# Optimization experiments

Hardware: AMD Instinct MI355X
Metric: run time of the kernel (lower is better)

The kernel has to match this reference:

```python
import jax, jax.numpy as jnp
import numpy as np

N_NODES = 100000
N_EDGES = 1600000
D_FEAT = 64


def setup_inputs() -> dict:
    key = jax.random.key(0)
    k1, k2, k3, k4 = jax.random.split(key, 4)
    x = jax.random.normal(k1, (N_NODES, D_FEAT), dtype=jnp.float32)
    edge_values = jax.random.uniform(k2, (N_EDGES,), dtype=jnp.float32)
    # row-sorted targets mimic a coalesced sparse COO matrix
    target_index = jnp.sort(jax.random.randint(k3, (N_EDGES,), 0, N_NODES, dtype=jnp.int32))
    source_index = jax.random.randint(k4, (N_EDGES,), 0, N_NODES, dtype=jnp.int32)
    return {"x": x, "edge_values": edge_values,
            "target_index": target_index, "source_index": source_index}


def reference(x, edge_values, target_index, source_index):
    # sparsify_message: gather source rows -> [n_edges, d]
    msg = x[source_index]
    # scale by sparse neighborhood values
    msg = edge_values[:, None] * msg
    # aggregate: scatter-sum into target cells -> [n_nodes, d]
    out = jax.ops.segment_sum(msg, target_index, num_segments=N_NODES)
    return out
```

## Files before the change

kernel.cpp:

```cpp
#include <hip/hip_runtime.h>

#define N_NODES 100000
#define N_EDGES 1600000
#define D_FEAT 64

__global__ __launch_bounds__(256) void build_row_ptr(
    const int* __restrict__ tgt, int* __restrict__ row_ptr)
{
    int e = blockIdx.x * blockDim.x + threadIdx.x;
    if (e >= N_EDGES) return;
    int cur = tgt[e];
    int lo  = (e == 0) ? 0 : tgt[e - 1] + 1;
    for (int n = lo; n <= cur; ++n) row_ptr[n] = e;
    if (e == N_EDGES - 1) {
        for (int n = cur + 1; n <= N_NODES; ++n) row_ptr[n] = N_EDGES;
    }
}

__global__ __launch_bounds__(256) void gather_sum(
    const float4* __restrict__ x4,
    const float*  __restrict__ ev,
    const int*    __restrict__ src,
    const int*    __restrict__ row_ptr,
    float4*       __restrict__ out4)
{
    const int node = blockIdx.x * 4 + (threadIdx.x >> 6);
    if (node >= N_NODES) return;
    const int lane = threadIdx.x & 63;
    const int g    = lane >> 4;
    const int f    = lane & 15;

    const int start = row_ptr[node];
    const int end   = row_ptr[node + 1];

    float4 acc = make_float4(0.f, 0.f, 0.f, 0.f);
    for (int e0 = start; e0 < end; e0 += 4) {
        const int  e     = e0 + g;
        const bool valid = (e < end);
        const int  es    = valid ? e : start;
        const float w    = valid ? ev[es] : 0.0f;
        const int   s    = src[es];
        const float4 v   = x4[s * 16 + f];
        acc.x = fmaf(w, v.x, acc.x);
        acc.y = fmaf(w, v.y, acc.y);
        acc.z = fmaf(w, v.z, acc.z);
        acc.w = fmaf(w, v.w, acc.w);
    }

    acc.x += __shfl_xor(acc.x, 16, 64);
    acc.y += __shfl_xor(acc.y, 16, 64);
    acc.z += __shfl_xor(acc.z, 16, 64);
    acc.w += __shfl_xor(acc.w, 16, 64);
    acc.x += __shfl_xor(acc.x, 32, 64);
    acc.y += __shfl_xor(acc.y, 32, 64);
    acc.z += __shfl_xor(acc.z, 32, 64);
    acc.w += __shfl_xor(acc.w, 32, 64);

    if (g == 0) out4[node * 16 + f] = acc;
}

extern "C" void kernel_launch(void* const* d_in, const int* in_sizes, int n_in,
                              void* d_out, int out_size, void* d_ws, size_t ws_size,
                              hipStream_t stream) {
    const float* x            = (const float*)d_in[0];
    const float* edge_values  = (const float*)d_in[1];
    const int*   target_index = (const int*)d_in[2];
    const int*   source_index = (const int*)d_in[3];
    float*       out          = (float*)d_out;
    int*         row_ptr      = (int*)d_ws;

    build_row_ptr<<<(N_EDGES + 255) / 256, 256, 0, stream>>>(target_index, row_ptr);

    gather_sum<<<(N_NODES + 3) / 4, 256, 0, stream>>>(
        (const float4*)x, edge_values, source_index, row_ptr, (float4*)out);
}
```

Baseline: 148.0 us.

## Process four nodes per 16-lane group with software-pipelined triple-buffered gathers

Each 16-lane group now handles four consecutive nodes as one contiguous edge range, walking the edges serially and flushing accumulators at row boundaries instead of splitting each node's edges across four lane groups and reducing with shuffles. Source indices, weights and x rows are prefetched two stages ahead in a rotating A/B/C register pipeline to hide gather latency. This removes the cross-lane shuffle reduction and the idle lanes on short rows. In exchange it raises register pressure and makes each group's work sequential, so per-thread memory parallelism depends on the prefetch depth.

```diff
diff --git a/kernel.cpp b/kernel.cpp
--- a/kernel.cpp
+++ b/kernel.cpp
@@ -24,39 +24,84 @@
     const int*    __restrict__ row_ptr,
     float4*       __restrict__ out4)
 {
-    const int node = blockIdx.x * 4 + (threadIdx.x >> 6);
-    if (node >= N_NODES) return;
-    const int lane = threadIdx.x & 63;
-    const int g    = lane >> 4;
-    const int f    = lane & 15;
+    const int gid = (blockIdx.x * 256 + threadIdx.x) >> 4;
+    if (gid >= N_NODES / 4) return;
+    const int f  = threadIdx.x & 15;
+    const int n0 = gid * 4;
 
-    const int start = row_ptr[node];
-    const int end   = row_ptr[node + 1];
+    const int rp0 = row_ptr[n0];
+    const int rp1 = row_ptr[n0 + 1];
+    const int rp2 = row_ptr[n0 + 2];
+    const int rp3 = row_ptr[n0 + 3];
+    const int rp4 = row_ptr[n0 + 4];
+
+    const int e0   = rp0;
+    const int eend = rp4;
+    const int len  = eend - e0;
 
     float4 acc = make_float4(0.f, 0.f, 0.f, 0.f);
-    for (int e0 = start; e0 < end; e0 += 4) {
-        const int  e     = e0 + g;
-        const bool valid = (e < end);
-        const int  es    = valid ? e : start;
-        const float w    = valid ? ev[es] : 0.0f;
-        const int   s    = src[es];
-        const float4 v   = x4[s * 16 + f];
-        acc.x = fmaf(w, v.x, acc.x);
-        acc.y = fmaf(w, v.y, acc.y);
-        acc.z = fmaf(w, v.z, acc.z);
-        acc.w = fmaf(w, v.w, acc.w);
+    int node  = n0;
+    int bound = rp1;
+
+    if (len > 0) {
+        const int emax = eend - 1;
+
+#define LOADSW(EIDX, S, W) do { int _e = (EIDX); int _ec = _e < emax ? _e : emax; \
+        S = src[_ec]; float _w = ev[_ec]; W = (_e < eend) ? _w : 0.0f; } while (0)
+
+#define CONSUME1(EIDX, W, X) do { int _ce = (EIDX); \
+        while (_ce < eend && _ce >= bound) { \
+            out4[node * 16 + f] = acc; \
+            acc = make_float4(0.f, 0.f, 0.f, 0.f); \
+            ++node; int _d = node - n0; \
+            bound = (_d == 1) ? rp2 : (_d == 2) ? rp3 : rp4; } \
+        acc.x = fmaf((W), (X).x, acc.x); \
+        acc.y = fmaf((W), (X).y, acc.y); \
+        acc.z = fmaf((W), (X).z, acc.z); \
+        acc.w = fmaf((W), (X).w, acc.w); } while (0)
+
+        int    sA0,sA1,sA2,sA3, sB0,sB1,sB2,sB3, sC0,sC1,sC2,sC3;
+        float  wA0,wA1,wA2,wA3, wB0,wB1,wB2,wB3, wC0,wC1,wC2,wC3;
+        float4 xA0,xA1,xA2,xA3, xB0,xB1,xB2,xB3, xC0,xC1,xC2,xC3;
+
+        LOADSW(e0 + 0, sA0, wA0); LOADSW(e0 + 1, sA1, wA1);
+        LOADSW(e0 + 2, sA2, wA2); LOADSW(e0 + 3, sA3, wA3);
+        LOADSW(e0 + 4, sB0, wB0); LOADSW(e0 + 5, sB1, wB1);
+        LOADSW(e0 + 6, sB2, wB2); LOADSW(e0 + 7, sB3, wB3);
+        xA0 = x4[sA0 * 16 + f]; xA1 = x4[sA1 * 16 + f];
+        xA2 = x4[sA2 * 16 + f]; xA3 = x4[sA3 * 16 + f];
+
+        for (int i = 0; i < len; i += 12) {
+            LOADSW(e0 + i + 8,  sC0, wC0); LOADSW(e0 + i + 9,  sC1, wC1);
+            LOADSW(e0 + i + 10, sC2, wC2); LOADSW(e0 + i + 11, sC3, wC3);
+            xB0 = x4[sB0 * 16 + f]; xB1 = x4[sB1 * 16 + f];
+            xB2 = x4[sB2 * 16 + f]; xB3 = x4[sB3 * 16 + f];
+            CONSUME1(e0 + i + 0, wA0, xA0); CONSUME1(e0 + i + 1, wA1, xA1);
+            CONSUME1(e0 + i + 2, wA2, xA2); CONSUME1(e0 + i + 3, wA3, xA3);
+
+            LOADSW(e0 + i + 12, sA0, wA0); LOADSW(e0 + i + 13, sA1, wA1);
+            LOADSW(e0 + i + 14, sA2, wA2); LOADSW(e0 + i + 15, sA3, wA3);
+            xC0 = x4[sC0 * 16 + f]; xC1 = x4[sC1 * 16 + f];
+            xC2 = x4[sC2 * 16 + f]; xC3 = x4[sC3 * 16 + f];
+            CONSUME1(e0 + i + 4, wB0, xB0); CONSUME1(e0 + i + 5, wB1, xB1);
+            CONSUME1(e0 + i + 6, wB2, xB2); CONSUME1(e0 + i + 7, wB3, xB3);
+
+            LOADSW(e0 + i + 16, sB0, wB0); LOADSW(e0 + i + 17, sB1, wB1);
+            LOADSW(e0 + i + 18, sB2, wB2); LOADSW(e0 + i + 19, sB3, wB3);
+            xA0 = x4[sA0 * 16 + f]; xA1 = x4[sA1 * 16 + f];
+            xA2 = x4[sA2 * 16 + f]; xA3 = x4[sA3 * 16 + f];
+            CONSUME1(e0 + i + 8,  wC0, xC0); CONSUME1(e0 + i + 9,  wC1, xC1);
+            CONSUME1(e0 + i + 10, wC2, xC2); CONSUME1(e0 + i + 11, wC3, xC3);
+        }
+#undef LOADSW
+#undef CONSUME1
     }
 
-    acc.x += __shfl_xor(acc.x, 16, 64);
-    acc.y += __shfl_xor(acc.y, 16, 64);
-    acc.z += __shfl_xor(acc.z, 16, 64);
-    acc.w += __shfl_xor(acc.w, 16, 64);
-    acc.x += __shfl_xor(acc.x, 32, 64);
-    acc.y += __shfl_xor(acc.y, 32, 64);
-    acc.z += __shfl_xor(acc.z, 32, 64);
-    acc.w += __shfl_xor(acc.w, 32, 64);
-
-    if (g == 0) out4[node * 16 + f] = acc;
+    while (node < n0 + 4) {
+        out4[node * 16 + f] = acc;
+        acc = make_float4(0.f, 0.f, 0.f, 0.f);
+        ++node;
+    }
 }
 
 extern "C" void kernel_launch(void* const* d_in, const int* in_sizes, int n_in,
@@ -71,6 +116,8 @@
 
     build_row_ptr<<<(N_EDGES + 255) / 256, 256, 0, stream>>>(target_index, row_ptr);
 
-    gather_sum<<<(N_NODES + 3) / 4, 256, 0, stream>>>(
+    const int n_groups = N_NODES / 4;
+    const int n_blocks = (n_groups + 15) / 16;
+    gather_sum<<<n_blocks, 256, 0, stream>>>(
         (const float4*)x, edge_values, source_index, row_ptr, (float4*)out);
 }
```

Measured after the change: 145.5 us. About the same (-1.7%).
